# Optimization experiments

Hardware: AMD Instinct MI355X
Metric: run time of the kernel (lower is better)

## Reference

```python
import jax, jax.numpy as jnp
import numpy as np

NUM_USERS = 100000
NUM_ITEMS = 50000
N_NODES = NUM_USERS + NUM_ITEMS
N_EDGES = 2_000_000
D = 64          # embedding_dim
HEADS = 4
F1 = D // HEADS  # per-head out dim of gat1
BATCH = 16384
NEG_SLOPE = 0.2  # PyG GATConv default negative_slope


def setup_inputs() -> dict:
    key = jax.random.key(0)
    ks = jax.random.split(key, 13)
    inp = {}
    inp["edge_index"] = jax.random.randint(ks[0], (2, N_EDGES), 0, N_NODES, dtype=jnp.int64)
    inp["batch_user_idx"] = jax.random.randint(ks[1], (BATCH,), 0, NUM_USERS, dtype=jnp.int64)
    inp["batch_item_idx"] = jax.random.randint(ks[2], (BATCH,), 0, NUM_ITEMS, dtype=jnp.int64)
    # Embedding tables (nn.init.normal_ std=0.01)
    inp["user_emb"] = 0.01 * jax.random.normal(ks[3], (NUM_USERS, D), dtype=jnp.float32)
    inp["item_emb"] = 0.01 * jax.random.normal(ks[4], (NUM_ITEMS, D), dtype=jnp.float32)
    # gat1: GATConv(64, 16, heads=4, concat=True)
    inp["W1"] = jax.random.normal(ks[5], (D, HEADS * F1), dtype=jnp.float32) / np.sqrt(D)
    inp["a_src1"] = jax.random.normal(ks[6], (HEADS, F1), dtype=jnp.float32) / np.sqrt(F1)
    inp["a_dst1"] = jax.random.normal(ks[7], (HEADS, F1), dtype=jnp.float32) / np.sqrt(F1)
    inp["b1"] = jnp.zeros((HEADS * F1,), dtype=jnp.float32)
    # gat2: GATConv(64, 64, heads=1)
    inp["W2"] = jax.random.normal(ks[8], (D, D), dtype=jnp.float32) / np.sqrt(D)
    inp["a_src2"] = jax.random.normal(ks[9], (1, D), dtype=jnp.float32) / np.sqrt(D)
    inp["a_dst2"] = jax.random.normal(ks[10], (1, D), dtype=jnp.float32) / np.sqrt(D)
    inp["b2"] = jnp.zeros((D,), dtype=jnp.float32)
    return inp


def _gat_conv(x, src, dst, W, a_src, a_dst, b, num_nodes):
    """PyG GATConv (eval mode, concat, self-loops already in src/dst)."""
    H, F = a_src.shape
    h = (x @ W).reshape(num_nodes, H, F)                 # [N,H,F]
    alpha_s = jnp.einsum('nhf,hf->nh', h, a_src)         # [N,H]
    alpha_d = jnp.einsum('nhf,hf->nh', h, a_dst)
    e = alpha_s[src] + alpha_d[dst]                      # [E,H]
    e = jax.nn.leaky_relu(e, NEG_SLOPE)
    # scatter-softmax over destination neighborhoods
    m = jax.ops.segment_max(e, dst, num_segments=num_nodes)   # [N,H]
    e = jnp.exp(e - m[dst])
    denom = jax.ops.segment_sum(e, dst, num_segments=num_nodes)
    alpha = e / denom[dst]                               # [E,H]
    msg = h[src] * alpha[:, :, None]                     # [E,H,F]
    agg = jax.ops.segment_sum(msg, dst, num_segments=num_nodes)  # [N,H,F]
    return agg.reshape(num_nodes, H * F) + b


def reference(user_emb, item_emb, W1, a_src1, a_dst1, b1,
              W2, a_src2, a_dst2, b2,
              edge_index, batch_user_idx, batch_item_idx):
    x = jnp.concatenate([user_emb, item_emb], axis=0)    # [N,D]
    n = x.shape[0]
    loop = jnp.arange(n, dtype=edge_index.dtype)          # add_self_loops=True
    src = jnp.concatenate([edge_index[0], loop])
    dst = jnp.concatenate([edge_index[1], loop])
    x = jax.nn.elu(_gat_conv(x, src, dst, W1, a_src1, a_dst1, b1, n))
    x = jax.nn.elu(_gat_conv(x, src, dst, W2, a_src2, a_dst2, b2, n))
    u = x[batch_user_idx]
    v = x[batch_item_idx + NUM_USERS]
    return jax.nn.sigmoid(jnp.sum(u * v, axis=1))        # [BATCH]
```

## Files before the change

### kernel.cpp

```cpp
#include <hip/hip_runtime.h>
#include <math.h>

#define SHIFT 8
#define NBMAX 1024
#define CAP   4096
#define TILE  16384
#define HSCALE 64.0f

typedef float v2f __attribute__((ext_vector_type(2)));
typedef short bf16x8 __attribute__((ext_vector_type(8)));
typedef float f32x4 __attribute__((ext_vector_type(4)));

__device__ __forceinline__ unsigned short f2bf(float f) {
    unsigned u = __float_as_uint(f);
    unsigned r = u + 0x7FFFu + ((u >> 16) & 1u);
    return (unsigned short)(r >> 16);
}
__device__ __forceinline__ unsigned pack2bf(float lo, float hi) {
    return (unsigned)f2bf(lo) | ((unsigned)f2bf(hi) << 16);
}
__device__ __forceinline__ float bflo(unsigned u) { return __uint_as_float(u << 16); }
__device__ __forceinline__ float bfhi(unsigned u) { return __uint_as_float(u & 0xFFFF0000u); }


__global__ void k_prep_w(const float* __restrict__ W1, const float* __restrict__ W2,
                         unsigned short* __restrict__ WT1, unsigned short* __restrict__ WT2,
                         unsigned* __restrict__ gcur, int NB) {
    int t = blockIdx.x * 256 + threadIdx.x;
    if (t < 4096) {
        int n = t & 63, k = t >> 6;
        WT1[n * 64 + k] = f2bf(W1[k * 64 + n]);
        WT2[n * 64 + k] = f2bf(W2[k * 64 + n]);
    }
    if (t < NB) gcur[t] = (unsigned)t * CAP;
}


__global__ __launch_bounds__(512) void k_partition(
    const int* __restrict__ src, const int* __restrict__ dst, int E,
    unsigned* __restrict__ gcur, unsigned* __restrict__ pairs, int NB) {
    __shared__ unsigned lh[NBMAX];
    __shared__ unsigned lcur[NBMAX];
    int t = threadIdx.x;
    for (int q = t; q < NB; q += 512) lh[q] = 0;
    __syncthreads();
    int base = blockIdx.x * TILE;
    int end = min(E, base + TILE);
    for (int i = base + t; i < end; i += 512)
        atomicAdd(&lh[((unsigned)dst[i]) >> SHIFT], 1u);
    __syncthreads();
    for (int q = t; q < NB; q += 512) {
        unsigned c = lh[q];
        lcur[q] = c ? atomicAdd(&gcur[q], c) : 0u;
    }
    __syncthreads();
    for (int i = base + t; i < end; i += 512) {
        unsigned d = (unsigned)dst[i];
        unsigned pos = atomicAdd(&lcur[d >> SHIFT], 1u);
        pairs[pos] = ((d & 255u) << 18) | (unsigned)src[i];
    }
}

__global__ __launch_bounds__(512) void k_bucket_sort(
    const unsigned* __restrict__ pairs, const unsigned* __restrict__ gcur,
    unsigned* __restrict__ beg, unsigned* __restrict__ endd,
    int* __restrict__ srt, int N, int NB) {
    __shared__ unsigned lh[256];
    __shared__ unsigned lcur[256];
    __shared__ unsigned sh[256];
    __shared__ int ssrt[CAP];
    int b = blockIdx.x;
    int t = threadIdx.x;
    unsigned s0 = (unsigned)b * CAP;
    int cnt = (int)(gcur[b] - s0);
    if (t < 256) lh[t] = 0;
    __syncthreads();
    for (int i = t; i < cnt; i += 512)
        atomicAdd(&lh[pairs[s0 + i] >> 18], 1u);
    __syncthreads();
    unsigned deg_t = 0;
    if (t < 256) { deg_t = lh[t]; sh[t] = deg_t; }
    __syncthreads();
    for (int off = 1; off < 256; off <<= 1) {
        unsigned x = 0;
        if (t < 256 && t >= off) x = sh[t - off];
        __syncthreads();
        if (t < 256) sh[t] += x;
        __syncthreads();
    }
    if (t < 256) {
        unsigned excl = sh[t] - deg_t;
        lcur[t] = excl;
        int node = (b << SHIFT) + t;
        if (node < N) { beg[node] = s0 + excl; endd[node] = s0 + excl + deg_t; }
    }
    __syncthreads();
    for (int i = t; i < cnt; i += 512) {
        unsigned pk = pairs[s0 + i];
        unsigned p = atomicAdd(&lcur[pk >> 18], 1u);
        ssrt[p] = (int)(pk & 0x3FFFFu);
    }
    __syncthreads();
    for (int i = t; i < cnt; i += 512) srt[s0 + i] = ssrt[i];
}


template <int HT, int BIN>
__global__ __launch_bounds__(256) void k_linear_mfma(
    const void* __restrict__ xav, const void* __restrict__ xbv, int split,
    const unsigned short* __restrict__ WTg,
    const float* __restrict__ a_src, const float* __restrict__ a_dst,
    unsigned char* __restrict__ h, float* __restrict__ as_out,
    float* __restrict__ ad_out, int N) {
    __shared__ unsigned short sX[64 * 72];
    __shared__ unsigned short sWT[64 * 72];
    __shared__ float sH[64 * 68];
    int t = threadIdx.x;
    int nodeBase = blockIdx.x * 64;

    {
        int r = t >> 2, c4 = (t & 3) * 16;
        int n = nodeBase + r;
        uint4 A = {0,0,0,0}, Bv = {0,0,0,0};
        if (BIN) {
            if (n < N) {
                const unsigned short* row = (const unsigned short*)xav + (size_t)n * 64 + c4;
                A  = ((const uint4*)(const void*)row)[0];
                Bv = ((const uint4*)(const void*)row)[1];
            }
        } else {
            float4 v0 = {0,0,0,0}, v1 = {0,0,0,0}, v2 = {0,0,0,0}, v3 = {0,0,0,0};
            if (n < N) {
                const float* row = (n < split) ? ((const float*)xav + (size_t)n * 64 + c4)
                                               : ((const float*)xbv + (size_t)(n - split) * 64 + c4);
                const float4* r4 = (const float4*)row;
                v0 = r4[0]; v1 = r4[1]; v2 = r4[2]; v3 = r4[3];
            }
            A  = make_uint4(pack2bf(v0.x, v0.y), pack2bf(v0.z, v0.w),
                            pack2bf(v1.x, v1.y), pack2bf(v1.z, v1.w));
            Bv = make_uint4(pack2bf(v2.x, v2.y), pack2bf(v2.z, v2.w),
                            pack2bf(v3.x, v3.y), pack2bf(v3.z, v3.w));
        }
        *(uint4*)(void*)(sX + r * 72 + c4) = A;
        *(uint4*)(void*)(sX + r * 72 + c4 + 8) = Bv;
        const uint4* wsrc = (const uint4*)(const void*)WTg;
        int base = (r * 64 + c4) >> 3;
        *(uint4*)(void*)(sWT + r * 72 + c4) = wsrc[base];
        *(uint4*)(void*)(sWT + r * 72 + c4 + 8) = wsrc[base + 1];
    }
    __syncthreads();

    {
        int lane = t & 63, w = t >> 6;
        int gl = lane & 15, quad = lane >> 4;
        int m0 = w * 16;
        const bf16x8 a0 = *(const bf16x8*)(void*)(sX + (m0 + gl) * 72 + quad * 8);
        const bf16x8 a1 = *(const bf16x8*)(void*)(sX + (m0 + gl) * 72 + 32 + quad * 8);
        f32x4 acc[4];
#pragma unroll
        for (int tt = 0; tt < 4; ++tt) {
            const bf16x8 b0 = *(const bf16x8*)(void*)(sWT + (tt * 16 + gl) * 72 + quad * 8);
            const bf16x8 b1 = *(const bf16x8*)(void*)(sWT + (tt * 16 + gl) * 72 + 32 + quad * 8);
            f32x4 c = {0.f, 0.f, 0.f, 0.f};
            c = __builtin_amdgcn_mfma_f32_16x16x32_bf16(a0, b0, c, 0, 0, 0);
            c = __builtin_amdgcn_mfma_f32_16x16x32_bf16(a1, b1, c, 0, 0, 0);
            acc[tt] = c;
        }
#pragma unroll
        for (int tt = 0; tt < 4; ++tt)
#pragma unroll
            for (int rr = 0; rr < 4; ++rr)
                sH[(m0 + quad * 4 + rr) * 68 + tt * 16 + gl] = acc[tt][rr];
    }
    __syncthreads();

    {
        int m = t >> 2, p = t & 3;
        int n = nodeBase + m;
        const float4* sp = (const float4*)(void*)(sH + m * 68 + p * 16);
        float4 q0 = sp[0], q1 = sp[1], q2 = sp[2], q3 = sp[3];
        float hv[16] = {q0.x,q0.y,q0.z,q0.w, q1.x,q1.y,q1.z,q1.w,
                        q2.x,q2.y,q2.z,q2.w, q3.x,q3.y,q3.z,q3.w};
        if (n < N) {
            unsigned dwords[4];
#pragma unroll
            for (int q = 0; q < 4; ++q) {
                int d0 = __builtin_amdgcn_cvt_pk_fp8_f32(hv[4*q] * HSCALE, hv[4*q+1] * HSCALE, 0, false);
                d0 = __builtin_amdgcn_cvt_pk_fp8_f32(hv[4*q+2] * HSCALE, hv[4*q+3] * HSCALE, d0, true);
                dwords[q] = (unsigned)d0;
            }
            ((uint4*)h)[(size_t)n * 4 + p] = make_uint4(dwords[0], dwords[1], dwords[2], dwords[3]);
            float ps = 0.f, pd = 0.f;
#pragma unroll
            for (int i = 0; i < 16; ++i) {
                ps = fmaf(hv[i], a_src[p * 16 + i], ps);
                pd = fmaf(hv[i], a_dst[p * 16 + i], pd);
            }
            if (HT == 4) {
                as_out[n * 4 + p] = ps;
                ad_out[n * 4 + p] = pd;
            } else {
                ps += __shfl_xor(ps, 1, 64); ps += __shfl_xor(ps, 2, 64);
                pd += __shfl_xor(pd, 1, 64); pd += __shfl_xor(pd, 2, 64);
                if (p == 0) { as_out[n] = ps; ad_out[n] = pd; }
            }
        }
    }
}

template <int HT>
__global__ void k_gat(const int* __restrict__ srt, const unsigned* __restrict__ beg,
                      const unsigned* __restrict__ endd,
                      const unsigned* __restrict__ hq, const float* __restrict__ as,
                      const float* __restrict__ ad, const float* __restrict__ b,
                      unsigned* __restrict__ xout, int N) {
    int lane = threadIdx.x & 63;
    int wid = (int)((blockIdx.x * blockDim.x + threadIdx.x) >> 6);
    int gl = lane & 15;
    int d = wid * 4 + (lane >> 4);
    bool active = d < N;
    const int hh = (HT == 4) ? (gl >> 2) : 0;
    float adv = 0.f, l = 0.f;
    float a0 = 0.f, a1 = 0.f, a2 = 0.f, a3 = 0.f;
    int kb = 0, end = 0;
    if (active) {
        adv = ad[d * HT + hh];
        float e0 = as[d * HT + hh] + adv;
        e0 = (e0 > 0.f) ? e0 : 0.2f * e0;
        float w0 = __expf(e0);
        unsigned dw = hq[(size_t)d * 16 + gl];
        v2f lo = __builtin_amdgcn_cvt_pk_f32_fp8((int)dw, false);
        v2f hi = __builtin_amdgcn_cvt_pk_f32_fp8((int)dw, true);
        l = w0;
        a0 = w0 * lo.x; a1 = w0 * lo.y; a2 = w0 * hi.x; a3 = w0 * hi.y;
        kb = (int)beg[d];
        end = (int)endd[d];
    }
    while (__ballot(kb < end)) {
        int idx = kb + gl;
        int ms = (active && idx < end) ? srt[idx] : 0;
        for (int i = 0; i < 16; ++i) {
            bool valid = active && (kb + i < end);
            if (!__ballot(valid)) break;
            int s = __shfl(ms, (lane & 48) + i, 64);
            if (valid) {
                float e = as[s * HT + hh] + adv;
                e = (e > 0.f) ? e : 0.2f * e;
                float w = __expf(e);
                unsigned dw = hq[(size_t)s * 16 + gl];
                v2f lo = __builtin_amdgcn_cvt_pk_f32_fp8((int)dw, false);
                v2f hi = __builtin_amdgcn_cvt_pk_f32_fp8((int)dw, true);
                l += w;
                a0 = fmaf(w, lo.x, a0);
                a1 = fmaf(w, lo.y, a1);
                a2 = fmaf(w, hi.x, a2);
                a3 = fmaf(w, hi.y, a3);
            }
        }
        kb += 16;
    }
    if (active) {
        float4 bb = ((const float4*)b)[gl];
        float rs = 1.f / (l * HSCALE);
        float v0 = a0 * rs + bb.x;
        float v1 = a1 * rs + bb.y;
        float v2 = a2 * rs + bb.z;
        float v3 = a3 * rs + bb.w;
        float o0 = (v0 > 0.f) ? v0 : expm1f(v0);
        float o1 = (v1 > 0.f) ? v1 : expm1f(v1);
        float o2 = (v2 > 0.f) ? v2 : expm1f(v2);
        float o3 = (v3 > 0.f) ? v3 : expm1f(v3);
        ((uint2*)xout)[(size_t)d * 16 + gl] = make_uint2(pack2bf(o0, o1), pack2bf(o2, o3));
    }
}

__global__ void k_dot_sig(const uint2* __restrict__ x2, const int* __restrict__ uidx,
                          const int* __restrict__ vidx, float* __restrict__ out,
                          int batch, int numUsers) {
    int lane = threadIdx.x & 63;
    int gl = lane & 15;
    int q = (int)(((blockIdx.x * blockDim.x + threadIdx.x) >> 6) * 4 + (lane >> 4));
    if (q >= batch) return;
    int u = uidx[q];
    int v = vidx[q] + numUsers;
    uint2 a = x2[(size_t)u * 16 + gl];
    uint2 c = x2[(size_t)v * 16 + gl];
    float p = bflo(a.x) * bflo(c.x) + bfhi(a.x) * bfhi(c.x)
            + bflo(a.y) * bflo(c.y) + bfhi(a.y) * bfhi(c.y);
#pragma unroll
    for (int off = 1; off < 16; off <<= 1) p += __shfl_xor(p, off, 64);
    if (gl == 0) out[q] = 1.f / (1.f + __expf(-p));
}


static inline int cdiv(long long a, long long b) { return (int)((a + b - 1) / b); }

extern "C" void kernel_launch(void* const* d_in, const int* in_sizes, int n_in,
                              void* d_out, int out_size, void* d_ws, size_t ws_size,
                              hipStream_t stream) {
    const int* edge_index = (const int*)d_in[0];
    const int* buidx      = (const int*)d_in[1];
    const int* biidx      = (const int*)d_in[2];
    const float* user_emb = (const float*)d_in[3];
    const float* item_emb = (const float*)d_in[4];
    const float* W1     = (const float*)d_in[5];
    const float* a_src1 = (const float*)d_in[6];
    const float* a_dst1 = (const float*)d_in[7];
    const float* b1     = (const float*)d_in[8];
    const float* W2     = (const float*)d_in[9];
    const float* a_src2 = (const float*)d_in[10];
    const float* a_dst2 = (const float*)d_in[11];
    const float* b2     = (const float*)d_in[12];
    float* out = (float*)d_out;

    const int E  = in_sizes[0] / 2;
    const int B  = in_sizes[1];
    const int NU = in_sizes[3] / 64;
    const int NI = in_sizes[4] / 64;
    const int N  = NU + NI;
    const int NB = cdiv(N, 1 << SHIFT);

    const int* src = edge_index;
    const int* dst = edge_index + E;

    float* ws = (float*)d_ws;
    size_t off = 0;
    unsigned* x_buf  = (unsigned*)(ws + off); off += (size_t)N * 32;
    unsigned* h_buf  = (unsigned*)(ws + off); off += (size_t)N * 16;
    float*    as_b   = ws + off; off += (size_t)N * 4;
    float*    ad_b   = ws + off; off += (size_t)N * 4;
    unsigned* gcur_b = (unsigned*)(ws + off); off += NBMAX;
    unsigned* beg_b  = (unsigned*)(ws + off); off += (size_t)N;
    unsigned* end_b  = (unsigned*)(ws + off); off += (size_t)N;
    unsigned* pairs_b= (unsigned*)(ws + off); off += (size_t)NB * CAP;
    int*      srt_b  = (int*)(ws + off); off += (size_t)NB * CAP;
    unsigned short* wt1_b = (unsigned short*)(ws + off); off += 2048;
    unsigned short* wt2_b = (unsigned short*)(ws + off); off += 2048;

    const int BS = 256;

    k_prep_w<<<16, BS, 0, stream>>>(W1, W2, wt1_b, wt2_b, gcur_b, NB);
    k_partition<<<cdiv(E, TILE), 512, 0, stream>>>(src, dst, E, gcur_b, pairs_b, NB);
    k_bucket_sort<<<NB, 512, 0, stream>>>(pairs_b, gcur_b, beg_b, end_b, srt_b, N, NB);

    k_linear_mfma<4, 0><<<cdiv(N, 64), BS, 0, stream>>>(user_emb, item_emb, NU, wt1_b,
                                                        a_src1, a_dst1,
                                                        (unsigned char*)h_buf, as_b, ad_b, N);
    k_gat<4><<<cdiv((long long)N * 16, BS), BS, 0, stream>>>(
        srt_b, beg_b, end_b, h_buf, as_b, ad_b, b1, x_buf, N);

    k_linear_mfma<1, 1><<<cdiv(N, 64), BS, 0, stream>>>(x_buf, x_buf, N, wt2_b,
                                                        a_src2, a_dst2,
                                                        (unsigned char*)h_buf, as_b, ad_b, N);
    k_gat<1><<<cdiv((long long)N * 16, BS), BS, 0, stream>>>(
        srt_b, beg_b, end_b, h_buf, as_b, ad_b, b2, x_buf, N);

    k_dot_sig<<<cdiv((long long)B * 16, BS), BS, 0, stream>>>(
        (const uint2*)x_buf, buidx, biidx, out, B, NU);
}
```

Before: 299.5 us.

## Fuse edge partition with layer-1 linear and drop weight-prep kernel

Merges the edge bucketing pass and the first MFMA linear transform into one launch, where the first blocks partition edges and the rest compute projections, so the two independent stages can overlap. The separate weight transpose kernel is removed: each linear block now converts and transposes W into shared memory itself, and the bucket cursors are zeroed with a memset and indexed relative to each bucket. The partition tile and block size are halved to fit the shared layout, which adds more global atomics and redundant per-block weight conversion with strided LDS stores.

Result: no change. 301.2 us (+0.5%).

```diff
diff --git a/kernel.cpp b/kernel.cpp
--- a/kernel.cpp
+++ b/kernel.cpp
@@ -4,8 +4,9 @@
 #define SHIFT 8
 #define NBMAX 1024
 #define CAP   4096
-#define TILE  16384
+#define TILE  8192
 #define HSCALE 64.0f
+#define SMEMB 35840
 
 typedef float v2f __attribute__((ext_vector_type(2)));
 typedef short bf16x8 __attribute__((ext_vector_type(8)));
@@ -23,42 +24,164 @@
 __device__ __forceinline__ float bfhi(unsigned u) { return __uint_as_float(u & 0xFFFF0000u); }
 
 
-__global__ void k_prep_w(const float* __restrict__ W1, const float* __restrict__ W2,
-                         unsigned short* __restrict__ WT1, unsigned short* __restrict__ WT2,
-                         unsigned* __restrict__ gcur, int NB) {
-    int t = blockIdx.x * 256 + threadIdx.x;
-    if (t < 4096) {
-        int n = t & 63, k = t >> 6;
-        WT1[n * 64 + k] = f2bf(W1[k * 64 + n]);
-        WT2[n * 64 + k] = f2bf(W2[k * 64 + n]);
-    }
-    if (t < NB) gcur[t] = (unsigned)t * CAP;
-}
-
-
-__global__ __launch_bounds__(512) void k_partition(
+__device__ __forceinline__ void partition_body(
+    char* smem, int bid,
     const int* __restrict__ src, const int* __restrict__ dst, int E,
     unsigned* __restrict__ gcur, unsigned* __restrict__ pairs, int NB) {
-    __shared__ unsigned lh[NBMAX];
-    __shared__ unsigned lcur[NBMAX];
+    unsigned* lh   = (unsigned*)smem;
+    unsigned* lcur = (unsigned*)(smem + 4096);
     int t = threadIdx.x;
-    for (int q = t; q < NB; q += 512) lh[q] = 0;
-    __syncthreads();
-    int base = blockIdx.x * TILE;
+    for (int q = t; q < NB; q += 256) lh[q] = 0;
+    __syncthreads();
+    int base = bid * TILE;
     int end = min(E, base + TILE);
-    for (int i = base + t; i < end; i += 512)
+    for (int i = base + t; i < end; i += 256)
         atomicAdd(&lh[((unsigned)dst[i]) >> SHIFT], 1u);
     __syncthreads();
-    for (int q = t; q < NB; q += 512) {
+    for (int q = t; q < NB; q += 256) {
         unsigned c = lh[q];
         lcur[q] = c ? atomicAdd(&gcur[q], c) : 0u;
     }
     __syncthreads();
-    for (int i = base + t; i < end; i += 512) {
+    for (int i = base + t; i < end; i += 256) {
         unsigned d = (unsigned)dst[i];
-        unsigned pos = atomicAdd(&lcur[d >> SHIFT], 1u);
-        pairs[pos] = ((d & 255u) << 18) | (unsigned)src[i];
-    }
+        unsigned bk = d >> SHIFT;
+        unsigned pos = atomicAdd(&lcur[bk], 1u);
+        pairs[(size_t)bk * CAP + pos] = ((d & 255u) << 18) | (unsigned)src[i];
+    }
+}
+
+template <int HT, int BIN>
+__device__ __forceinline__ void linear_body(
+    char* smem, int bid,
+    const void* __restrict__ xav, const void* __restrict__ xbv, int split,
+    const float* __restrict__ W,
+    const float* __restrict__ a_src, const float* __restrict__ a_dst,
+    unsigned char* __restrict__ h, float* __restrict__ as_out,
+    float* __restrict__ ad_out, int N) {
+    unsigned short* sX  = (unsigned short*)smem;
+    unsigned short* sWT = (unsigned short*)(smem + 9216);
+    float*          sH  = (float*)(smem + 18432);
+    int t = threadIdx.x;
+    int nodeBase = bid * 64;
+
+    {
+        int r = t >> 2, c4 = (t & 3) * 16;
+        int n = nodeBase + r;
+        uint4 A = {0,0,0,0}, Bv = {0,0,0,0};
+        if (BIN) {
+            if (n < N) {
+                const unsigned short* row = (const unsigned short*)xav + (size_t)n * 64 + c4;
+                A  = ((const uint4*)(const void*)row)[0];
+                Bv = ((const uint4*)(const void*)row)[1];
+            }
+        } else {
+            float4 v0 = {0,0,0,0}, v1 = {0,0,0,0}, v2 = {0,0,0,0}, v3 = {0,0,0,0};
+            if (n < N) {
+                const float* row = (n < split) ? ((const float*)xav + (size_t)n * 64 + c4)
+                                               : ((const float*)xbv + (size_t)(n - split) * 64 + c4);
+                const float4* r4 = (const float4*)row;
+                v0 = r4[0]; v1 = r4[1]; v2 = r4[2]; v3 = r4[3];
+            }
+            A  = make_uint4(pack2bf(v0.x, v0.y), pack2bf(v0.z, v0.w),
+                            pack2bf(v1.x, v1.y), pack2bf(v1.z, v1.w));
+            Bv = make_uint4(pack2bf(v2.x, v2.y), pack2bf(v2.z, v2.w),
+                            pack2bf(v3.x, v3.y), pack2bf(v3.z, v3.w));
+        }
+        *(uint4*)(void*)(sX + r * 72 + c4) = A;
+        *(uint4*)(void*)(sX + r * 72 + c4 + 8) = Bv;
+        int kk = r;
+        const float4* w4 = (const float4*)(W + (size_t)kk * 64 + c4);
+        float4 w0 = w4[0], w1 = w4[1], w2 = w4[2], w3 = w4[3];
+        float wf[16] = {w0.x,w0.y,w0.z,w0.w, w1.x,w1.y,w1.z,w1.w,
+                        w2.x,w2.y,w2.z,w2.w, w3.x,w3.y,w3.z,w3.w};
+#pragma unroll
+        for (int i = 0; i < 16; ++i) sWT[(c4 + i) * 72 + kk] = f2bf(wf[i]);
+    }
+    __syncthreads();
+
+    {
+        int lane = t & 63, w = t >> 6;
+        int gl = lane & 15, quad = lane >> 4;
+        int m0 = w * 16;
+        const bf16x8 a0 = *(const bf16x8*)(void*)(sX + (m0 + gl) * 72 + quad * 8);
+        const bf16x8 a1 = *(const bf16x8*)(void*)(sX + (m0 + gl) * 72 + 32 + quad * 8);
+        f32x4 acc[4];
+#pragma unroll
+        for (int tt = 0; tt < 4; ++tt) {
+            const bf16x8 b0 = *(const bf16x8*)(void*)(sWT + (tt * 16 + gl) * 72 + quad * 8);
+            const bf16x8 b1 = *(const bf16x8*)(void*)(sWT + (tt * 16 + gl) * 72 + 32 + quad * 8);
+            f32x4 c = {0.f, 0.f, 0.f, 0.f};
+            c = __builtin_amdgcn_mfma_f32_16x16x32_bf16(a0, b0, c, 0, 0, 0);
+            c = __builtin_amdgcn_mfma_f32_16x16x32_bf16(a1, b1, c, 0, 0, 0);
+            acc[tt] = c;
+        }
+#pragma unroll
+        for (int tt = 0; tt < 4; ++tt)
+#pragma unroll
+            for (int rr = 0; rr < 4; ++rr)
+                sH[(m0 + quad * 4 + rr) * 68 + tt * 16 + gl] = acc[tt][rr];
+    }
+    __syncthreads();
+
+    {
+        int m = t >> 2, p = t & 3;
+        int n = nodeBase + m;
+        const float4* sp = (const float4*)(void*)(sH + m * 68 + p * 16);
+        float4 q0 = sp[0], q1 = sp[1], q2 = sp[2], q3 = sp[3];
+        float hv[16] = {q0.x,q0.y,q0.z,q0.w, q1.x,q1.y,q1.z,q1.w,
+                        q2.x,q2.y,q2.z,q2.w, q3.x,q3.y,q3.z,q3.w};
+        if (n < N) {
+            unsigned dwords[4];
+#pragma unroll
+            for (int q = 0; q < 4; ++q) {
+                int d0 = __builtin_amdgcn_cvt_pk_fp8_f32(hv[4*q] * HSCALE, hv[4*q+1] * HSCALE, 0, false);
+                d0 = __builtin_amdgcn_cvt_pk_fp8_f32(hv[4*q+2] * HSCALE, hv[4*q+3] * HSCALE, d0, true);
+                dwords[q] = (unsigned)d0;
+            }
+            ((uint4*)h)[(size_t)n * 4 + p] = make_uint4(dwords[0], dwords[1], dwords[2], dwords[3]);
+            float ps = 0.f, pd = 0.f;
+#pragma unroll
+            for (int i = 0; i < 16; ++i) {
+                ps = fmaf(hv[i], a_src[p * 16 + i], ps);
+                pd = fmaf(hv[i], a_dst[p * 16 + i], pd);
+            }
+            if (HT == 4) {
+                as_out[n * 4 + p] = ps;
+                ad_out[n * 4 + p] = pd;
+            } else {
+                ps += __shfl_xor(ps, 1, 64); ps += __shfl_xor(ps, 2, 64);
+                pd += __shfl_xor(pd, 1, 64); pd += __shfl_xor(pd, 2, 64);
+                if (p == 0) { as_out[n] = ps; ad_out[n] = pd; }
+            }
+        }
+    }
+}
+
+
+__global__ __launch_bounds__(256) void k_part_lin1(
+    const int* __restrict__ src, const int* __restrict__ dst, int E,
+    unsigned* __restrict__ gcur, unsigned* __restrict__ pairs, int NB, int PB,
+    const float* __restrict__ xa, const float* __restrict__ xb, int split,
+    const float* __restrict__ W1,
+    const float* __restrict__ a_src, const float* __restrict__ a_dst,
+    unsigned char* __restrict__ h, float* __restrict__ as_out,
+    float* __restrict__ ad_out, int N) {
+    __shared__ char smem[SMEMB];
+    if ((int)blockIdx.x < PB)
+        partition_body(smem, blockIdx.x, src, dst, E, gcur, pairs, NB);
+    else
+        linear_body<4, 0>(smem, blockIdx.x - PB, xa, xb, split, W1,
+                          a_src, a_dst, h, as_out, ad_out, N);
+}
+
+__global__ __launch_bounds__(256) void k_linear2(
+    const void* __restrict__ xav, const float* __restrict__ W,
+    const float* __restrict__ a_src, const float* __restrict__ a_dst,
+    unsigned char* __restrict__ h, float* __restrict__ as_out,
+    float* __restrict__ ad_out, int N) {
+    __shared__ char smem[SMEMB];
+    linear_body<1, 1>(smem, blockIdx.x, xav, xav, N, W, a_src, a_dst, h, as_out, ad_out, N);
 }
 
 __global__ __launch_bounds__(512) void k_bucket_sort(
@@ -72,7 +195,7 @@
     int b = blockIdx.x;
     int t = threadIdx.x;
     unsigned s0 = (unsigned)b * CAP;
-    int cnt = (int)(gcur[b] - s0);
+    int cnt = (int)gcur[b];
     if (t < 256) lh[t] = 0;
     __syncthreads();
     for (int i = t; i < cnt; i += 512)
@@ -102,110 +225,6 @@
     }
     __syncthreads();
     for (int i = t; i < cnt; i += 512) srt[s0 + i] = ssrt[i];
-}
-
-
-template <int HT, int BIN>
-__global__ __launch_bounds__(256) void k_linear_mfma(
-    const void* __restrict__ xav, const void* __restrict__ xbv, int split,
-    const unsigned short* __restrict__ WTg,
-    const float* __restrict__ a_src, const float* __restrict__ a_dst,
-    unsigned char* __restrict__ h, float* __restrict__ as_out,
-    float* __restrict__ ad_out, int N) {
-    __shared__ unsigned short sX[64 * 72];
-    __shared__ unsigned short sWT[64 * 72];
-    __shared__ float sH[64 * 68];
-    int t = threadIdx.x;
-    int nodeBase = blockIdx.x * 64;
-
-    {
-        int r = t >> 2, c4 = (t & 3) * 16;
-        int n = nodeBase + r;
-        uint4 A = {0,0,0,0}, Bv = {0,0,0,0};
-        if (BIN) {
-            if (n < N) {
-                const unsigned short* row = (const unsigned short*)xav + (size_t)n * 64 + c4;
-                A  = ((const uint4*)(const void*)row)[0];
-                Bv = ((const uint4*)(const void*)row)[1];
-            }
-        } else {
-            float4 v0 = {0,0,0,0}, v1 = {0,0,0,0}, v2 = {0,0,0,0}, v3 = {0,0,0,0};
-            if (n < N) {
-                const float* row = (n < split) ? ((const float*)xav + (size_t)n * 64 + c4)
-                                               : ((const float*)xbv + (size_t)(n - split) * 64 + c4);
-                const float4* r4 = (const float4*)row;
-                v0 = r4[0]; v1 = r4[1]; v2 = r4[2]; v3 = r4[3];
-            }
-            A  = make_uint4(pack2bf(v0.x, v0.y), pack2bf(v0.z, v0.w),
-                            pack2bf(v1.x, v1.y), pack2bf(v1.z, v1.w));
-            Bv = make_uint4(pack2bf(v2.x, v2.y), pack2bf(v2.z, v2.w),
-                            pack2bf(v3.x, v3.y), pack2bf(v3.z, v3.w));
-        }
-        *(uint4*)(void*)(sX + r * 72 + c4) = A;
-        *(uint4*)(void*)(sX + r * 72 + c4 + 8) = Bv;
-        const uint4* wsrc = (const uint4*)(const void*)WTg;
-        int base = (r * 64 + c4) >> 3;
-        *(uint4*)(void*)(sWT + r * 72 + c4) = wsrc[base];
-        *(uint4*)(void*)(sWT + r * 72 + c4 + 8) = wsrc[base + 1];
-    }
-    __syncthreads();
-
-    {
-        int lane = t & 63, w = t >> 6;
-        int gl = lane & 15, quad = lane >> 4;
-        int m0 = w * 16;
-        const bf16x8 a0 = *(const bf16x8*)(void*)(sX + (m0 + gl) * 72 + quad * 8);
-        const bf16x8 a1 = *(const bf16x8*)(void*)(sX + (m0 + gl) * 72 + 32 + quad * 8);
-        f32x4 acc[4];
-#pragma unroll
-        for (int tt = 0; tt < 4; ++tt) {
-            const bf16x8 b0 = *(const bf16x8*)(void*)(sWT + (tt * 16 + gl) * 72 + quad * 8);
-            const bf16x8 b1 = *(const bf16x8*)(void*)(sWT + (tt * 16 + gl) * 72 + 32 + quad * 8);
-            f32x4 c = {0.f, 0.f, 0.f, 0.f};
-            c = __builtin_amdgcn_mfma_f32_16x16x32_bf16(a0, b0, c, 0, 0, 0);
-            c = __builtin_amdgcn_mfma_f32_16x16x32_bf16(a1, b1, c, 0, 0, 0);
-            acc[tt] = c;
-        }
-#pragma unroll
-        for (int tt = 0; tt < 4; ++tt)
-#pragma unroll
-            for (int rr = 0; rr < 4; ++rr)
-                sH[(m0 + quad * 4 + rr) * 68 + tt * 16 + gl] = acc[tt][rr];
-    }
-    __syncthreads();
-
-    {
-        int m = t >> 2, p = t & 3;
-        int n = nodeBase + m;
-        const float4* sp = (const float4*)(void*)(sH + m * 68 + p * 16);
-        float4 q0 = sp[0], q1 = sp[1], q2 = sp[2], q3 = sp[3];
-        float hv[16] = {q0.x,q0.y,q0.z,q0.w, q1.x,q1.y,q1.z,q1.w,
-                        q2.x,q2.y,q2.z,q2.w, q3.x,q3.y,q3.z,q3.w};
-        if (n < N) {
-            unsigned dwords[4];
-#pragma unroll
-            for (int q = 0; q < 4; ++q) {
-                int d0 = __builtin_amdgcn_cvt_pk_fp8_f32(hv[4*q] * HSCALE, hv[4*q+1] * HSCALE, 0, false);
-                d0 = __builtin_amdgcn_cvt_pk_fp8_f32(hv[4*q+2] * HSCALE, hv[4*q+3] * HSCALE, d0, true);
-                dwords[q] = (unsigned)d0;
-            }
-            ((uint4*)h)[(size_t)n * 4 + p] = make_uint4(dwords[0], dwords[1], dwords[2], dwords[3]);
-            float ps = 0.f, pd = 0.f;
-#pragma unroll
-            for (int i = 0; i < 16; ++i) {
-                ps = fmaf(hv[i], a_src[p * 16 + i], ps);
-                pd = fmaf(hv[i], a_dst[p * 16 + i], pd);
-            }
-            if (HT == 4) {
-                as_out[n * 4 + p] = ps;
-                ad_out[n * 4 + p] = pd;
-            } else {
-                ps += __shfl_xor(ps, 1, 64); ps += __shfl_xor(ps, 2, 64);
-                pd += __shfl_xor(pd, 1, 64); pd += __shfl_xor(pd, 2, 64);
-                if (p == 0) { as_out[n] = ps; ad_out[n] = pd; }
-            }
-        }
-    }
 }
 
 template <int HT>
@@ -319,6 +338,8 @@
     const int NI = in_sizes[4] / 64;
     const int N  = NU + NI;
     const int NB = cdiv(N, 1 << SHIFT);
+    const int PB = cdiv(E, TILE);
+    const int LB = cdiv(N, 64);
 
     const int* src = edge_index;
     const int* dst = edge_index + E;
@@ -334,24 +355,22 @@
     unsigned* end_b  = (unsigned*)(ws + off); off += (size_t)N;
     unsigned* pairs_b= (unsigned*)(ws + off); off += (size_t)NB * CAP;
     int*      srt_b  = (int*)(ws + off); off += (size_t)NB * CAP;
-    unsigned short* wt1_b = (unsigned short*)(ws + off); off += 2048;
-    unsigned short* wt2_b = (unsigned short*)(ws + off); off += 2048;
 
     const int BS = 256;
 
-    k_prep_w<<<16, BS, 0, stream>>>(W1, W2, wt1_b, wt2_b, gcur_b, NB);
-    k_partition<<<cdiv(E, TILE), 512, 0, stream>>>(src, dst, E, gcur_b, pairs_b, NB);
+    hipMemsetAsync(gcur_b, 0, NBMAX * sizeof(unsigned), stream);
+
+    k_part_lin1<<<PB + LB, BS, 0, stream>>>(src, dst, E, gcur_b, pairs_b, NB, PB,
+                                            user_emb, item_emb, NU, W1, a_src1, a_dst1,
+                                            (unsigned char*)h_buf, as_b, ad_b, N);
+
     k_bucket_sort<<<NB, 512, 0, stream>>>(pairs_b, gcur_b, beg_b, end_b, srt_b, N, NB);
 
-    k_linear_mfma<4, 0><<<cdiv(N, 64), BS, 0, stream>>>(user_emb, item_emb, NU, wt1_b,
-                                                        a_src1, a_dst1,
-                                                        (unsigned char*)h_buf, as_b, ad_b, N);
     k_gat<4><<<cdiv((long long)N * 16, BS), BS, 0, stream>>>(
         srt_b, beg_b, end_b, h_buf, as_b, ad_b, b1, x_buf, N);
 
-    k_linear_mfma<1, 1><<<cdiv(N, 64), BS, 0, stream>>>(x_buf, x_buf, N, wt2_b,
-                                                        a_src2, a_dst2,
-                                                        (unsigned char*)h_buf, as_b, ad_b, N);
+    k_linear2<<<LB, BS, 0, stream>>>(x_buf, W2, a_src2, a_dst2,
+                                     (unsigned char*)h_buf, as_b, ad_b, N);
     k_gat<1><<<cdiv((long long)N * 16, BS), BS, 0, stream>>>(
         srt_b, beg_b, end_b, h_buf, as_b, ad_b, b2, x_buf, N);
 
```
